# Kernel optimization log

Measured on AMD Instinct MI355X. Metric: run time of the kernel, lower is better.

## Reference

```python
import jax, jax.numpy as jnp
import numpy as np

EPS = 1e-5

def _bn(z, g, b):
    # train-mode BatchNorm2d: batch stats over (B,H,W), biased variance
    mean = z.mean(axis=(0, 2, 3), keepdims=True)
    var = z.var(axis=(0, 2, 3), keepdims=True)
    return g[None, :, None, None] * (z - mean) * jax.lax.rsqrt(var + EPS) + b[None, :, None, None]

def _conv1x1(x, w):
    # x: [B,C,H,W], w: [O,C] -> [B,O,H,W]
    return jnp.einsum('bchw,oc->bohw', x, w)

def _proj(x, w1, g1, b1, w2, g2, b2):
    z = _bn(_conv1x1(x, w1), g1, b1)
    return _bn(_conv1x1(z, w2), g2, b2)

def setup_inputs() -> dict:
    key = jax.random.key(0)
    ks = jax.random.split(key, 24)
    B, Cx, Cy, M, H, W = 4, 512, 256, 64, 64, 64
    f32 = jnp.float32
    def wmat(k, o, c):
        return jax.random.normal(k, (o, c), f32) * (c ** -0.5)
    def gamma(k, c):
        return 1.0 + 0.1 * jax.random.normal(k, (c,), f32)
    def beta(k, c):
        return 0.1 * jax.random.normal(k, (c,), f32)
    inp = {
        'x': jax.random.normal(ks[0], (B, Cx, H, W), f32),
        'y': jax.random.normal(ks[1], (B, Cy, H, W), f32),
        # f_self
        'ws1': wmat(ks[2], M, Cx), 'gs1': gamma(ks[3], M), 'bs1': beta(ks[4], M),
        'ws2': wmat(ks[5], M, M),  'gs2': gamma(ks[6], M), 'bs2': beta(ks[7], M),
        # f_x
        'wx1': wmat(ks[8], M, Cx), 'gx1': gamma(ks[9], M), 'bx1': beta(ks[10], M),
        'wx2': wmat(ks[11], M, M), 'gx2': gamma(ks[12], M), 'bx2': beta(ks[13], M),
        # f_y
        'wy1': wmat(ks[14], M, Cy), 'gy1': gamma(ks[15], M), 'by1': beta(ks[16], M),
        'wy2': wmat(ks[17], M, M),  'gy2': gamma(ks[18], M), 'by2': beta(ks[19], M),
        # f_up
        'wu': wmat(ks[20], Cx, M), 'gu': gamma(ks[21], Cx), 'bu': beta(ks[22], Cx),
    }
    return inp

def reference(x, y, ws1, gs1, bs1, ws2, gs2, bs2,
              wx1, gx1, bx1, wx2, gx2, bx2,
              wy1, gy1, by1, wy2, gy2, by2,
              wu, gu, bu):
    B, C, H, W = x.shape
    M = ws1.shape[0]
    N = H * W
    fself = _proj(x, ws1, gs1, bs1, ws2, gs2, bs2).reshape(B, M, N).transpose(0, 2, 1)  # [B,N,M]
    fx = _proj(x, wx1, gx1, bx1, wx2, gx2, bx2).reshape(B, M, N).transpose(0, 2, 1)      # [B,N,M]
    fy = _proj(y, wy1, gy1, by1, wy2, gy2, by2).reshape(B, M, N)                          # [B,M,N]
    sim = jnp.matmul(fx, fy)                  # [B,N,N]  (scale=False)
    attn = jax.nn.softmax(sim, axis=-1)
    fout = jnp.matmul(attn, fself)            # [B,N,M]
    fout = fout.transpose(0, 2, 1).reshape(B, M, H, W)
    out = _bn(_conv1x1(fout, wu), gu, bu)
    return x + out
```

## Files before the change

### kernel.cpp

```cpp
#include <hip/hip_runtime.h>
#include <hip/hip_fp16.h>
#include <cstdint>

constexpr int N_ = 4096;
constexpr float CNT = 16384.f;

typedef __attribute__((ext_vector_type(8))) _Float16 half8;
typedef __attribute__((ext_vector_type(4))) float f32x4;
union fragh { half8 h8; int i4[4]; };

__device__ inline int pkh(float a, float b) {
  union { __half2 h; int i; } u;
  u.h = __float22half2_rn(float2{a, b});
  return u.i;
}


__global__ __launch_bounds__(256) void prep1_k(const float* __restrict__ ws1,
                                               const float* __restrict__ wx1,
                                               const float* __restrict__ wy1,
                                               float* __restrict__ wt1) {
  int e = blockIdx.x * 256 + threadIdx.x;
  if (e < 32768) {
    int k = e >> 6, o = e & 63;
    wt1[e] = ws1[o * 512 + k];
  } else if (e < 65536) {
    int e2 = e - 32768;
    int k = e2 >> 6, o = e2 & 63;
    wt1[e] = wx1[o * 512 + k];
  } else {
    int e3 = e - 65536;
    int k = e3 >> 6, o = e3 & 63;
    wt1[e] = wy1[o * 256 + k];
  }
}

__global__ __launch_bounds__(256) void prep2_k(
    const float* __restrict__ ws2, const float* __restrict__ wx2,
    const float* __restrict__ wy2,
    const float* __restrict__ gs1, const float* __restrict__ bs1,
    const float* __restrict__ gx1, const float* __restrict__ bx1,
    const float* __restrict__ gy1, const float* __restrict__ by1,
    const float* __restrict__ stats, float* __restrict__ wt2) {
  const int branch = blockIdx.x;
  const int t = threadIdx.x;
  const float* W = branch == 0 ? ws2 : (branch == 1 ? wx2 : wy2);
  const float* g1 = branch == 0 ? gs1 : (branch == 1 ? gx1 : gy1);
  const float* b1 = branch == 0 ? bs1 : (branch == 1 ? bx1 : by1);
  const float* stin = stats + branch * 128;
  float* outW = wt2 + branch * 4096;
  float* outB = wt2 + 12288 + branch * 64;

#pragma unroll
  for (int i = 0; i < 16; ++i) {
    int e = i * 256 + t;
    int k = e >> 6, o = e & 63;
    float mean = stin[k] * (1.f / CNT);
    float var = stin[64 + k] * (1.f / CNT) - mean * mean;
    float sc = g1[k] * rsqrtf(var + 1e-5f);
    outW[e] = W[o * 64 + k] * sc;
  }
  if (t < 64) {
    float s = 0.f;
    for (int k = 0; k < 64; ++k) {
      float mean = stin[k] * (1.f / CNT);
      float var = stin[64 + k] * (1.f / CNT) - mean * mean;
      float sc = g1[k] * rsqrtf(var + 1e-5f);
      float sh = b1[k] - mean * sc;
      s += W[t * 64 + k] * sh;
    }
    outB[t] = s;
  }
}

__global__ __launch_bounds__(256) void prepu_k(const float* __restrict__ wu,
                                               float* __restrict__ wut) {
  int e = blockIdx.x * 256 + threadIdx.x;
  int k = e >> 9, o = e & 511;
  wut[e] = wu[o * 64 + k];
}


__global__ __launch_bounds__(256) void conv1_k(
    const float* __restrict__ x, const float* __restrict__ y,
    const float* __restrict__ wt1,
    float* __restrict__ z1s, float* __restrict__ z1x, float* __restrict__ z1y,
    float* __restrict__ stats) {
  const int t = threadIdx.x;
  const int b = blockIdx.x >> 4;
  const int n0 = (blockIdx.x & 15) * 256;
  const int branch = blockIdx.y;
  const float* A = branch == 2 ? y : x;
  const float* Wt = wt1 + (branch == 0 ? 0 : (branch == 1 ? 32768 : 65536));
  float* out = branch == 0 ? z1s : (branch == 1 ? z1x : z1y);
  const int K = branch == 2 ? 256 : 512;
  float* st = stats + branch * 128;

  __shared__ float sA[16][260];
  __shared__ float sW[16][68];

  const int ng4 = (t & 31) * 4;
  const int og8 = (t >> 5) * 8;
  float acc[8][8];
#pragma unroll
  for (int i = 0; i < 8; ++i)
#pragma unroll
    for (int j = 0; j < 8; ++j) acc[i][j] = 0.f;

  const float* Ap = A + ((size_t)b * K + (t >> 6)) * N_ + n0 + (t & 63) * 4;
  const float* Wp = Wt + (size_t)(t >> 4) * 64 + (t & 15) * 4;
  const int arow = t >> 6, acol = (t & 63) * 4;
  const int wrow = t >> 4, wcol = (t & 15) * 4;

  float4 pa[4];
  float4 pw;
#pragma unroll
  for (int i = 0; i < 4; ++i) pa[i] = *(const float4*)(Ap + (size_t)(4 * i) * N_);
  pw = *(const float4*)Wp;
  Ap += (size_t)16 * N_;
  Wp += 16 * 64;
#pragma unroll
  for (int i = 0; i < 4; ++i) *(float4*)&sA[arow + 4 * i][acol] = pa[i];
  *(float4*)&sW[wrow][wcol] = pw;
  __syncthreads();

#pragma unroll 1
  for (int k0 = 0; k0 < K; k0 += 16) {
    const bool more = (k0 + 16) < K;
    if (more) {
#pragma unroll
      for (int i = 0; i < 4; ++i) pa[i] = *(const float4*)(Ap + (size_t)(4 * i) * N_);
      pw = *(const float4*)Wp;
      Ap += (size_t)16 * N_;
      Wp += 16 * 64;
    }
#pragma unroll
    for (int k = 0; k < 16; ++k) {
      float4 a0 = *(const float4*)&sA[k][ng4];
      float4 a1 = *(const float4*)&sA[k][128 + ng4];
      float4 w0 = *(const float4*)&sW[k][og8];
      float4 w1 = *(const float4*)&sW[k][og8 + 4];
      float av[8] = {a0.x, a0.y, a0.z, a0.w, a1.x, a1.y, a1.z, a1.w};
      float wv[8] = {w0.x, w0.y, w0.z, w0.w, w1.x, w1.y, w1.z, w1.w};
#pragma unroll
      for (int i = 0; i < 8; ++i)
#pragma unroll
        for (int j = 0; j < 8; ++j) acc[i][j] = fmaf(wv[i], av[j], acc[i][j]);
    }
    __syncthreads();
    if (more) {
#pragma unroll
      for (int i = 0; i < 4; ++i) *(float4*)&sA[arow + 4 * i][acol] = pa[i];
      *(float4*)&sW[wrow][wcol] = pw;
    }
    __syncthreads();
  }

  float* Cb = out + ((size_t)b * 64 + og8) * N_ + n0;
#pragma unroll
  for (int i = 0; i < 8; ++i) {
    float4 v0 = {acc[i][0], acc[i][1], acc[i][2], acc[i][3]};
    float4 v1 = {acc[i][4], acc[i][5], acc[i][6], acc[i][7]};
    *(float4*)&Cb[(size_t)i * N_ + ng4] = v0;
    *(float4*)&Cb[(size_t)i * N_ + 128 + ng4] = v1;
  }
#pragma unroll
  for (int i = 0; i < 8; ++i) {
    float s = 0.f, q = 0.f;
#pragma unroll
    for (int j = 0; j < 8; ++j) { s += acc[i][j]; q += acc[i][j] * acc[i][j]; }
#pragma unroll
    for (int d = 1; d < 32; d <<= 1) { s += __shfl_xor(s, d); q += __shfl_xor(q, d); }
    if ((t & 31) == 0) { atomicAdd(&st[og8 + i], s); atomicAdd(&st[64 + og8 + i], q); }
  }
}

__global__ __launch_bounds__(256) void conv2_k(
    const float* __restrict__ z1s, const float* __restrict__ z1x,
    const float* __restrict__ z1y, const float* __restrict__ wt2,
    float* __restrict__ z2s, float* __restrict__ z2x, float* __restrict__ z2y,
    float* __restrict__ stats) {
  const int t = threadIdx.x;
  const int b = blockIdx.x >> 4;
  const int n0 = (blockIdx.x & 15) * 256;
  const int branch = blockIdx.y;
  const float* A = branch == 0 ? z1s : (branch == 1 ? z1x : z1y);
  const float* Wt = wt2 + branch * 4096;
  const float* bias = wt2 + 12288 + branch * 64;
  float* out = branch == 0 ? z2s : (branch == 1 ? z2x : z2y);
  float* st = stats + (3 + branch) * 128;

  __shared__ float sA[16][260];
  __shared__ float sW[16][68];

  const int ng4 = (t & 31) * 4;
  const int og8 = (t >> 5) * 8;
  float acc[8][8];
#pragma unroll
  for (int i = 0; i < 8; ++i) {
    float bi = bias[og8 + i];
#pragma unroll
    for (int j = 0; j < 8; ++j) acc[i][j] = bi;
  }

  const float* Ap = A + ((size_t)b * 64 + (t >> 6)) * N_ + n0 + (t & 63) * 4;
  const float* Wp = Wt + (size_t)(t >> 4) * 64 + (t & 15) * 4;
  const int arow = t >> 6, acol = (t & 63) * 4;
  const int wrow = t >> 4, wcol = (t & 15) * 4;

  float4 pa[4];
  float4 pw;
#pragma unroll
  for (int i = 0; i < 4; ++i) pa[i] = *(const float4*)(Ap + (size_t)(4 * i) * N_);
  pw = *(const float4*)Wp;
  Ap += (size_t)16 * N_;
  Wp += 16 * 64;
#pragma unroll
  for (int i = 0; i < 4; ++i) *(float4*)&sA[arow + 4 * i][acol] = pa[i];
  *(float4*)&sW[wrow][wcol] = pw;
  __syncthreads();

#pragma unroll 1
  for (int k0 = 0; k0 < 64; k0 += 16) {
    const bool more = (k0 + 16) < 64;
    if (more) {
#pragma unroll
      for (int i = 0; i < 4; ++i) pa[i] = *(const float4*)(Ap + (size_t)(4 * i) * N_);
      pw = *(const float4*)Wp;
      Ap += (size_t)16 * N_;
      Wp += 16 * 64;
    }
#pragma unroll
    for (int k = 0; k < 16; ++k) {
      float4 a0 = *(const float4*)&sA[k][ng4];
      float4 a1 = *(const float4*)&sA[k][128 + ng4];
      float4 w0 = *(const float4*)&sW[k][og8];
      float4 w1 = *(const float4*)&sW[k][og8 + 4];
      float av[8] = {a0.x, a0.y, a0.z, a0.w, a1.x, a1.y, a1.z, a1.w};
      float wv[8] = {w0.x, w0.y, w0.z, w0.w, w1.x, w1.y, w1.z, w1.w};
#pragma unroll
      for (int i = 0; i < 8; ++i)
#pragma unroll
        for (int j = 0; j < 8; ++j) acc[i][j] = fmaf(wv[i], av[j], acc[i][j]);
    }
    __syncthreads();
    if (more) {
#pragma unroll
      for (int i = 0; i < 4; ++i) *(float4*)&sA[arow + 4 * i][acol] = pa[i];
      *(float4*)&sW[wrow][wcol] = pw;
    }
    __syncthreads();
  }

  float* Cb = out + ((size_t)b * 64 + og8) * N_ + n0;
#pragma unroll
  for (int i = 0; i < 8; ++i) {
    float4 v0 = {acc[i][0], acc[i][1], acc[i][2], acc[i][3]};
    float4 v1 = {acc[i][4], acc[i][5], acc[i][6], acc[i][7]};
    *(float4*)&Cb[(size_t)i * N_ + ng4] = v0;
    *(float4*)&Cb[(size_t)i * N_ + 128 + ng4] = v1;
  }
#pragma unroll
  for (int i = 0; i < 8; ++i) {
    float s = 0.f, q = 0.f;
#pragma unroll
    for (int j = 0; j < 8; ++j) { s += acc[i][j]; q += acc[i][j] * acc[i][j]; }
#pragma unroll
    for (int d = 1; d < 32; d <<= 1) { s += __shfl_xor(s, d); q += __shfl_xor(q, d); }
    if ((t & 31) == 0) { atomicAdd(&st[og8 + i], s); atomicAdd(&st[64 + og8 + i], q); }
  }
}

__global__ __launch_bounds__(256) void pack_k(
    const float* __restrict__ z2s, const float* __restrict__ z2x,
    const float* __restrict__ z2y,
    const float* __restrict__ gs2, const float* __restrict__ bs2,
    const float* __restrict__ gx2, const float* __restrict__ bx2,
    const float* __restrict__ gy2, const float* __restrict__ by2,
    int* __restrict__ Qh, int* __restrict__ Kf, int* __restrict__ Vf,
    const float* __restrict__ stats) {
  const int job = blockIdx.z;
  const int idx = blockIdx.x * 256 + threadIdx.x;
  const float* z2 = job == 0 ? z2x : (job == 1 ? z2y : z2s);
  const float* g2 = job == 0 ? gx2 : (job == 1 ? gy2 : gs2);
  const float* b2 = job == 0 ? bx2 : (job == 1 ? by2 : bs2);
  const float* st = stats + (job == 0 ? 4 : (job == 1 ? 5 : 3)) * 128;
  int* outp = job == 0 ? Qh : (job == 1 ? Kf : Vf);

  auto snorm = [&](int c, float& s, float& h) {
    float mean = st[c] * (1.f / CNT);
    float var = st[64 + c] * (1.f / CNT) - mean * mean;
    float r = rsqrtf(var + 1e-5f);
    s = g2[c] * r;
    h = b2[c] - mean * s;
  };
  if (job == 0) {
    int n = idx & 4095, c = (idx >> 12) & 31, b = idx >> 17;
    float s0, h0, s1, h1;
    snorm(2 * c, s0, h0);
    snorm(2 * c + 1, s1, h1);
    float v0 = z2[((size_t)b * 64 + 2 * c) * N_ + n] * s0 + h0;
    float v1 = z2[((size_t)b * 64 + 2 * c + 1) * N_ + n] * s1 + h1;
    outp[idx] = pkh(v0, v1);
  } else if (job == 1) {
    int n = idx & 4095, c = (idx >> 12) & 31, b = idx >> 17;
    float s0, h0, s1, h1;
    snorm(2 * c, s0, h0);
    snorm(2 * c + 1, s1, h1);
    float v0 = z2[((size_t)b * 64 + 2 * c) * N_ + n] * s0 + h0;
    float v1 = z2[((size_t)b * 64 + 2 * c + 1) * N_ + n] * s1 + h1;
    int t16 = n >> 4, la = n & 15, g = c >> 4, quad = (c & 15) >> 2, jj = c & 3;
    outp[(((b * 256 + t16) * 2 + g) * 64 + quad * 16 + la) * 4 + jj] = pkh(v0, v1);
  } else {
    int k = idx & 2047, ch = (idx >> 11) & 63, b = idx >> 17;
    float s0, h0;
    snorm(ch, s0, h0);
    float2 v = *(const float2*)&z2[((size_t)b * 64 + ch) * N_ + 2 * k];
    int kb = k >> 4, p = k & 15, quad = p >> 2, w = p & 3, mt = ch >> 4, la = ch & 15;
    outp[(((b * 128 + kb) * 4 + mt) * 64 + quad * 16 + la) * 4 + w] =
        pkh(v.x * s0 + h0, v.y * s0 + h0);
  }
}

__global__ __launch_bounds__(256, 4) void attn_k(const int* __restrict__ Qh,
                                                 const int* __restrict__ Kf,
                                                 const int* __restrict__ Vf,
                                                 float* __restrict__ fout) {
  const int tid = threadIdx.x;
  const int lane = tid & 63;
  const int wid = tid >> 6;
  const int la = lane & 15;
  const int quad = lane >> 4;
  const int b = blockIdx.x & 3;
  const int qbase = (blockIdx.x >> 2) * 16;
  const int* Qb = Qh + (size_t)b * 32 * N_;
  const int* Kb4 = Kf + (size_t)b * 131072;
  const int* Vb4 = Vf + (size_t)b * 131072;

  __shared__ union USm {
    int P16[4][16 * 20];
    struct { float O[4][16][69]; float M[4][16]; float L[4][16]; } e;
  } smu;
  int* myP = smu.P16[wid];

  fragh aq[2];
#pragma unroll
  for (int c = 0; c < 2; ++c)
#pragma unroll
    for (int j = 0; j < 4; ++j)
      aq[c].i4[j] = Qb[(size_t)(c * 16 + quad * 4 + j) * N_ + qbase + la];

  f32x4 o[4];
  float mrun = -3.0e38f, lrun = 0.f;
#pragma unroll
  for (int mt = 0; mt < 4; ++mt) o[mt] = f32x4{0.f, 0.f, 0.f, 0.f};

  const int jbeg = wid * (N_ / 4);
  const int jend = jbeg + N_ / 4;

  int4 ka[2][2], kb2[2][2];
#pragma unroll
  for (int nt = 0; nt < 2; ++nt)
#pragma unroll
    for (int g = 0; g < 2; ++g)
      ka[nt][g] = *(const int4*)&Kb4[((((jbeg >> 4) + nt) * 2 + g) * 64 + lane) * 4];

  auto body = [&](int j0, int4 (&kc)[2][2], int4 (&kn)[2][2]) {
    f32x4 s[2];
#pragma unroll
    for (int nt = 0; nt < 2; ++nt) {
      fragh k0, k1;
      k0.i4[0] = kc[nt][0].x; k0.i4[1] = kc[nt][0].y;
      k0.i4[2] = kc[nt][0].z; k0.i4[3] = kc[nt][0].w;
      k1.i4[0] = kc[nt][1].x; k1.i4[1] = kc[nt][1].y;
      k1.i4[2] = kc[nt][1].z; k1.i4[3] = kc[nt][1].w;
      f32x4 z = f32x4{0.f, 0.f, 0.f, 0.f};
      z = __builtin_amdgcn_mfma_f32_16x16x32_f16(k0.h8, aq[0].h8, z, 0, 0, 0);
      s[nt] = __builtin_amdgcn_mfma_f32_16x16x32_f16(k1.h8, aq[1].h8, z, 0, 0, 0);
    }
    int4 vv[4];
#pragma unroll
    for (int mt = 0; mt < 4; ++mt)
      vv[mt] = *(const int4*)&Vb4[(((j0 >> 5) * 4 + mt) * 64 + lane) * 4];
    const int nj = (j0 + 32 < jend) ? (j0 + 32) : jbeg;
#pragma unroll
    for (int nt = 0; nt < 2; ++nt)
#pragma unroll
      for (int g = 0; g < 2; ++g)
        kn[nt][g] = *(const int4*)&Kb4[((((nj >> 4) + nt) * 2 + g) * 64 + lane) * 4];
    float t0 = fmaxf(fmaxf(s[0][0], s[0][1]), fmaxf(s[0][2], s[0][3]));
    float t1 = fmaxf(fmaxf(s[1][0], s[1][1]), fmaxf(s[1][2], s[1][3]));
    float t = fmaxf(t0, t1);
    t = fmaxf(t, __shfl_xor(t, 16));
    t = fmaxf(t, __shfl_xor(t, 32));
    float mnew = fmaxf(mrun, t);
    float alpha = __expf(mrun - mnew);
    float p[2][4];
    float ps = 0.f;
#pragma unroll
    for (int nt = 0; nt < 2; ++nt)
#pragma unroll
      for (int r = 0; r < 4; ++r) {
        p[nt][r] = __expf(s[nt][r] - mnew);
        ps += p[nt][r];
      }
    ps += __shfl_xor(ps, 16);
    ps += __shfl_xor(ps, 32);
    lrun = lrun * alpha + ps;
    mrun = mnew;
#pragma unroll
    for (int nt = 0; nt < 2; ++nt) {
      myP[(nt * 8 + quad * 2 + 0) * 20 + la] = pkh(p[nt][0], p[nt][1]);
      myP[(nt * 8 + quad * 2 + 1) * 20 + la] = pkh(p[nt][2], p[nt][3]);
    }
    __asm__ __volatile__("s_waitcnt lgkmcnt(0)" ::: "memory");
    fragh pb;
#pragma unroll
    for (int j = 0; j < 4; ++j) pb.i4[j] = myP[(quad * 4 + j) * 20 + la];
#pragma unroll
    for (int mt = 0; mt < 4; ++mt) {
      o[mt][0] *= alpha; o[mt][1] *= alpha;
      o[mt][2] *= alpha; o[mt][3] *= alpha;
    }
#pragma unroll
    for (int mt = 0; mt < 4; ++mt) {
      fragh vb;
      vb.i4[0] = vv[mt].x; vb.i4[1] = vv[mt].y;
      vb.i4[2] = vv[mt].z; vb.i4[3] = vv[mt].w;
      o[mt] = __builtin_amdgcn_mfma_f32_16x16x32_f16(vb.h8, pb.h8, o[mt], 0, 0, 0);
    }
  };

#pragma unroll 1
  for (int j0 = jbeg; j0 < jend; j0 += 64) {
    body(j0, ka, kb2);
    body(j0 + 32, kb2, ka);
  }

  __syncthreads();
  if (quad == 0) {
    smu.e.M[wid][la] = mrun;
    smu.e.L[wid][la] = lrun;
  }
#pragma unroll
  for (int mt = 0; mt < 4; ++mt)
#pragma unroll
    for (int r = 0; r < 4; ++r) smu.e.O[wid][la][mt * 16 + quad * 4 + r] = o[mt][r];
  __syncthreads();

#pragma unroll
  for (int t = 0; t < 4; ++t) {
    int oidx = t * 256 + tid;
    int m = oidx >> 4;
    int q = oidx & 15;
    float m0 = fmaxf(fmaxf(smu.e.M[0][q], smu.e.M[1][q]),
                     fmaxf(smu.e.M[2][q], smu.e.M[3][q]));
    float num = 0.f, den = 0.f;
#pragma unroll
    for (int w = 0; w < 4; ++w) {
      float wgt = __expf(smu.e.M[w][q] - m0);
      num += wgt * smu.e.O[w][q][m];
      den += wgt * smu.e.L[w][q];
    }
    fout[((size_t)b * 64 + m) * N_ + qbase + q] = num / den;
  }
}

__global__ __launch_bounds__(256) void convup_k(const float* __restrict__ fout,
                                                const float* __restrict__ wut,
                                                float* __restrict__ u,
                                                float* __restrict__ stats) {
  const int t = threadIdx.x;
  const int b = blockIdx.x >> 4;
  const int n0 = (blockIdx.x & 15) * 256;
  const int o0 = blockIdx.y * 64;

  __shared__ float sA[16][260];
  __shared__ float sW[16][68];

  const int ng4 = (t & 31) * 4;
  const int og8 = (t >> 5) * 8;
  float acc[8][8];
#pragma unroll
  for (int i = 0; i < 8; ++i)
#pragma unroll
    for (int j = 0; j < 8; ++j) acc[i][j] = 0.f;

  const float* Ap = fout + ((size_t)b * 64 + (t >> 6)) * N_ + n0 + (t & 63) * 4;
  const float* Wp = wut + (size_t)(t >> 4) * 512 + o0 + (t & 15) * 4;
  const int arow = t >> 6, acol = (t & 63) * 4;
  const int wrow = t >> 4, wcol = (t & 15) * 4;

  float4 pa[4];
  float4 pw;
#pragma unroll
  for (int i = 0; i < 4; ++i) pa[i] = *(const float4*)(Ap + (size_t)(4 * i) * N_);
  pw = *(const float4*)Wp;
  Ap += (size_t)16 * N_;
  Wp += 16 * 512;
#pragma unroll
  for (int i = 0; i < 4; ++i) *(float4*)&sA[arow + 4 * i][acol] = pa[i];
  *(float4*)&sW[wrow][wcol] = pw;
  __syncthreads();

#pragma unroll 1
  for (int k0 = 0; k0 < 64; k0 += 16) {
    const bool more = (k0 + 16) < 64;
    if (more) {
#pragma unroll
      for (int i = 0; i < 4; ++i) pa[i] = *(const float4*)(Ap + (size_t)(4 * i) * N_);
      pw = *(const float4*)Wp;
      Ap += (size_t)16 * N_;
      Wp += 16 * 512;
    }
#pragma unroll
    for (int k = 0; k < 16; ++k) {
      float4 a0 = *(const float4*)&sA[k][ng4];
      float4 a1 = *(const float4*)&sA[k][128 + ng4];
      float4 w0 = *(const float4*)&sW[k][og8];
      float4 w1 = *(const float4*)&sW[k][og8 + 4];
      float av[8] = {a0.x, a0.y, a0.z, a0.w, a1.x, a1.y, a1.z, a1.w};
      float wv[8] = {w0.x, w0.y, w0.z, w0.w, w1.x, w1.y, w1.z, w1.w};
#pragma unroll
      for (int i = 0; i < 8; ++i)
#pragma unroll
        for (int j = 0; j < 8; ++j) acc[i][j] = fmaf(wv[i], av[j], acc[i][j]);
    }
    __syncthreads();
    if (more) {
#pragma unroll
      for (int i = 0; i < 4; ++i) *(float4*)&sA[arow + 4 * i][acol] = pa[i];
      *(float4*)&sW[wrow][wcol] = pw;
    }
    __syncthreads();
  }

  float* Cb = u + ((size_t)b * 512 + o0 + og8) * N_ + n0;
#pragma unroll
  for (int i = 0; i < 8; ++i) {
    float4 v0 = {acc[i][0], acc[i][1], acc[i][2], acc[i][3]};
    float4 v1 = {acc[i][4], acc[i][5], acc[i][6], acc[i][7]};
    *(float4*)&Cb[(size_t)i * N_ + ng4] = v0;
    *(float4*)&Cb[(size_t)i * N_ + 128 + ng4] = v1;
  }
#pragma unroll
  for (int i = 0; i < 8; ++i) {
    float s = 0.f, q = 0.f;
#pragma unroll
    for (int j = 0; j < 8; ++j) { s += acc[i][j]; q += acc[i][j] * acc[i][j]; }
#pragma unroll
    for (int d = 1; d < 32; d <<= 1) { s += __shfl_xor(s, d); q += __shfl_xor(q, d); }
    if ((t & 31) == 0) {
      atomicAdd(&stats[768 + o0 + og8 + i], s);
      atomicAdd(&stats[1280 + o0 + og8 + i], q);
    }
  }
}

__global__ __launch_bounds__(256) void final_k(const float* __restrict__ x,
                                               const float* __restrict__ u,
                                               const float* __restrict__ gu,
                                               const float* __restrict__ bu,
                                               const float* __restrict__ stats,
                                               float* __restrict__ out) {
  size_t idx = (size_t)blockIdx.x * 256 + threadIdx.x;
  int c = (int)((idx >> 12) & 511);
  float mean = stats[768 + c] * (1.f / CNT);
  float var = stats[1280 + c] * (1.f / CNT) - mean * mean;
  float r = rsqrtf(var + 1e-5f);
  float s = gu[c] * r;
  float sh = bu[c] - mean * s;
  out[idx] = x[idx] + u[idx] * s + sh;
}

extern "C" void kernel_launch(void* const* d_in, const int* in_sizes, int n_in,
                              void* d_out, int out_size, void* d_ws, size_t ws_size,
                              hipStream_t stream) {
  const float* x = (const float*)d_in[0];
  const float* y = (const float*)d_in[1];
  const float* ws1 = (const float*)d_in[2];
  const float* gs1 = (const float*)d_in[3];
  const float* bs1 = (const float*)d_in[4];
  const float* ws2 = (const float*)d_in[5];
  const float* gs2 = (const float*)d_in[6];
  const float* bs2 = (const float*)d_in[7];
  const float* wx1 = (const float*)d_in[8];
  const float* gx1 = (const float*)d_in[9];
  const float* bx1 = (const float*)d_in[10];
  const float* wx2 = (const float*)d_in[11];
  const float* gx2 = (const float*)d_in[12];
  const float* bx2 = (const float*)d_in[13];
  const float* wy1 = (const float*)d_in[14];
  const float* gy1 = (const float*)d_in[15];
  const float* by1 = (const float*)d_in[16];
  const float* wy2 = (const float*)d_in[17];
  const float* gy2 = (const float*)d_in[18];
  const float* by2 = (const float*)d_in[19];
  const float* wu = (const float*)d_in[20];
  const float* gu = (const float*)d_in[21];
  const float* bu = (const float*)d_in[22];
  float* out = (float*)d_out;

  float* w = (float*)d_ws;
  const size_t M1 = 1048576;
  float* z1s = w + 0 * M1;
  float* z1x = w + 1 * M1;
  float* z1y = w + 2 * M1;
  float* z2s = w + 3 * M1;
  float* z2x = w + 4 * M1;
  float* z2y = w + 5 * M1;
  float* fout = w + 6 * M1;
  float* u = w + 7 * M1;
  int* Qh = (int*)(w + 15 * M1);
  int* Kf = Qh + 524288;
  int* Vf = Kf + 524288;
  float* stats = (float*)(Vf + 524288);
  float* wt1 = u;
  float* wt2 = fout;
  float* wut = z1s;

  hipMemsetAsync(stats, 0, 1792 * sizeof(float), stream);

  prep1_k<<<dim3(320), dim3(256), 0, stream>>>(ws1, wx1, wy1, wt1);
  conv1_k<<<dim3(64, 3), dim3(256), 0, stream>>>(x, y, wt1, z1s, z1x, z1y, stats);
  prep2_k<<<dim3(3), dim3(256), 0, stream>>>(ws2, wx2, wy2, gs1, bs1, gx1, bx1,
                                             gy1, by1, stats, wt2);
  conv2_k<<<dim3(64, 3), dim3(256), 0, stream>>>(z1s, z1x, z1y, wt2, z2s, z2x,
                                                 z2y, stats);
  prepu_k<<<dim3(128), dim3(256), 0, stream>>>(wu, wut);
  pack_k<<<dim3(2048, 1, 3), dim3(256), 0, stream>>>(z2s, z2x, z2y, gs2, bs2, gx2,
                                                     bx2, gy2, by2, Qh, Kf, Vf,
                                                     stats);
  attn_k<<<dim3(1024), dim3(256), 0, stream>>>(Qh, Kf, Vf, fout);
  convup_k<<<dim3(64, 8), dim3(256), 0, stream>>>(fout, wut, u, stats);
  final_k<<<dim3(32768), dim3(256), 0, stream>>>(x, u, gu, bu, stats, out);
}
```

Before: 378.6 us.

## Move 1x1 projection convs to split-fp16 MFMA with fragment-packed layouts

Rewrites conv1 and conv2 to use fp16 MFMA instructions. Each fp32 value is split into high and low half parts, and three MFMAs per tile stand in for the scalar FP32 FMA loop with LDS tiling. A new packA kernel converts x and y into MFMA fragment layout. Intermediates z1/z2 are stored as hi/lo half pairs in fragment order, so pack_k and attn_k now read Q and K in the new layout. This trades an extra packing pass over the inputs and the error of the hi/lo split for much higher matrix throughput in the projection GEMMs.

```diff
diff --git a/kernel.cpp b/kernel.cpp
--- a/kernel.cpp
+++ b/kernel.cpp
@@ -14,25 +14,70 @@
   u.h = __float22half2_rn(float2{a, b});
   return u.i;
 }
-
+__device__ inline void pk_hl(float a, float b, int& h, int& l) {
+  __half ah = __float2half_rn(a), bh = __float2half_rn(b);
+  union { __half2 v; int i; } u;
+  u.v = __halves2half2(ah, bh);
+  h = u.i;
+  float ar = a - __half2float(ah), br = b - __half2float(bh);
+  union { __half2 v; int i; } w2;
+  w2.v = __float22half2_rn(float2{ar, br});
+  l = w2.i;
+}
+__device__ inline float2 uph(int v) {
+  union { __half2 h; int i; } u;
+  u.i = v;
+  return float2{__half2float(__low2half(u.h)), __half2float(__high2half(u.h))};
+}
+
+
+__global__ __launch_bounds__(256) void packA_k(const float* __restrict__ x,
+                                               const float* __restrict__ y,
+                                               int* __restrict__ Afx,
+                                               int* __restrict__ Afy) {
+  const int job = blockIdx.y;
+  if (job == 1 && blockIdx.x >= 2048) return;
+  const int idx = blockIdx.x * 256 + threadIdx.x;
+  const float* src = job ? y : x;
+  int* dst = job ? Afy : Afx;
+  const int KT = job ? 8 : 16;
+  const int loOff = job ? 2097152 : 4194304;
+  const int n = idx & 4095, q = (idx >> 12) & 3;
+  const int kt = job ? ((idx >> 14) & 7) : ((idx >> 14) & 15);
+  const int b = job ? (idx >> 17) : (idx >> 18);
+  const float* sp = src + ((size_t)(b * (KT * 32) + kt * 32 + q * 8)) * N_ + n;
+  float a[8];
+#pragma unroll
+  for (int j = 0; j < 8; ++j) a[j] = sp[(size_t)j * N_];
+  int4 hi, lo;
+  pk_hl(a[0], a[1], hi.x, lo.x);
+  pk_hl(a[2], a[3], hi.y, lo.y);
+  pk_hl(a[4], a[5], hi.z, lo.z);
+  pk_hl(a[6], a[7], hi.w, lo.w);
+  const int base = (((b * KT + kt) * 256 + (n >> 4)) * 64 + q * 16 + (n & 15)) * 4;
+  *(int4*)&dst[base] = hi;
+  *(int4*)&dst[loOff + base] = lo;
+}
 
 __global__ __launch_bounds__(256) void prep1_k(const float* __restrict__ ws1,
                                                const float* __restrict__ wx1,
                                                const float* __restrict__ wy1,
-                                               float* __restrict__ wt1) {
-  int e = blockIdx.x * 256 + threadIdx.x;
-  if (e < 32768) {
-    int k = e >> 6, o = e & 63;
-    wt1[e] = ws1[o * 512 + k];
-  } else if (e < 65536) {
-    int e2 = e - 32768;
-    int k = e2 >> 6, o = e2 & 63;
-    wt1[e] = wx1[o * 512 + k];
-  } else {
-    int e3 = e - 65536;
-    int k = e3 >> 6, o = e3 & 63;
-    wt1[e] = wy1[o * 256 + k];
-  }
+                                               int* __restrict__ wt1f) {
+  const int idx = blockIdx.x * 256 + threadIdx.x;
+  const float* W;
+  int KT, K, hiBase, loOff, e;
+  if (idx < 16384) { W = ws1; KT = 16; K = 512; hiBase = 0; loOff = 16384; e = idx; }
+  else if (idx < 32768) { W = wx1; KT = 16; K = 512; hiBase = 32768; loOff = 16384; e = idx - 16384; }
+  else { W = wy1; KT = 8; K = 256; hiBase = 65536; loOff = 8192; e = idx - 32768; }
+  const int jj = e & 3, lane = (e >> 2) & 63;
+  int kt, ot;
+  if (KT == 16) { kt = (e >> 8) & 15; ot = e >> 12; } else { kt = (e >> 8) & 7; ot = e >> 11; }
+  const int o = ot * 16 + (lane & 15);
+  const int k = kt * 32 + (lane >> 4) * 8 + 2 * jj;
+  int h, l;
+  pk_hl(W[o * K + k], W[o * K + k + 1], h, l);
+  wt1f[hiBase + e] = h;
+  wt1f[hiBase + loOff + e] = l;
 }
 
 __global__ __launch_bounds__(256) void prep2_k(
@@ -41,24 +86,33 @@
     const float* __restrict__ gs1, const float* __restrict__ bs1,
     const float* __restrict__ gx1, const float* __restrict__ bx1,
     const float* __restrict__ gy1, const float* __restrict__ by1,
-    const float* __restrict__ stats, float* __restrict__ wt2) {
+    const float* __restrict__ stats, int* __restrict__ wt2f,
+    float* __restrict__ biasf) {
   const int branch = blockIdx.x;
   const int t = threadIdx.x;
   const float* W = branch == 0 ? ws2 : (branch == 1 ? wx2 : wy2);
   const float* g1 = branch == 0 ? gs1 : (branch == 1 ? gx1 : gy1);
   const float* b1 = branch == 0 ? bs1 : (branch == 1 ? bx1 : by1);
   const float* stin = stats + branch * 128;
-  float* outW = wt2 + branch * 4096;
-  float* outB = wt2 + 12288 + branch * 64;
-
-#pragma unroll
-  for (int i = 0; i < 16; ++i) {
-    int e = i * 256 + t;
-    int k = e >> 6, o = e & 63;
+  int* outW = wt2f + branch * 4096;
+
+  auto scale = [&](int k) {
     float mean = stin[k] * (1.f / CNT);
     float var = stin[64 + k] * (1.f / CNT) - mean * mean;
-    float sc = g1[k] * rsqrtf(var + 1e-5f);
-    outW[e] = W[o * 64 + k] * sc;
+    return g1[k] * rsqrtf(var + 1e-5f);
+  };
+#pragma unroll
+  for (int i = 0; i < 8; ++i) {
+    int e = i * 256 + t;
+    int jj = e & 3, lane = (e >> 2) & 63, kt = (e >> 8) & 1, ot = e >> 9;
+    int o = ot * 16 + (lane & 15);
+    int k = kt * 32 + (lane >> 4) * 8 + 2 * jj;
+    float w0 = W[o * 64 + k] * scale(k);
+    float w1 = W[o * 64 + k + 1] * scale(k + 1);
+    int h, l;
+    pk_hl(w0, w1, h, l);
+    outW[e] = h;
+    outW[2048 + e] = l;
   }
   if (t < 64) {
     float s = 0.f;
@@ -69,7 +123,7 @@
       float sh = b1[k] - mean * sc;
       s += W[t * 64 + k] * sh;
     }
-    outB[t] = s;
+    biasf[branch * 64 + t] = s;
   }
 }
 
@@ -80,212 +134,183 @@
   wut[e] = wu[o * 64 + k];
 }
 
-
 __global__ __launch_bounds__(256) void conv1_k(
-    const float* __restrict__ x, const float* __restrict__ y,
-    const float* __restrict__ wt1,
-    float* __restrict__ z1s, float* __restrict__ z1x, float* __restrict__ z1y,
+    const int* __restrict__ Afx, const int* __restrict__ Afy,
+    const int* __restrict__ wt1f, int* __restrict__ z1f,
     float* __restrict__ stats) {
   const int t = threadIdx.x;
+  const int lane = t & 63;
+  const int wv = t >> 6;
+  const int la = lane & 15;
+  const int quad = lane >> 4;
   const int b = blockIdx.x >> 4;
-  const int n0 = (blockIdx.x & 15) * 256;
+  const int ns = blockIdx.x & 15;
   const int branch = blockIdx.y;
-  const float* A = branch == 2 ? y : x;
-  const float* Wt = wt1 + (branch == 0 ? 0 : (branch == 1 ? 32768 : 65536));
-  float* out = branch == 0 ? z1s : (branch == 1 ? z1x : z1y);
-  const int K = branch == 2 ? 256 : 512;
+  const int KT = branch == 2 ? 8 : 16;
+  const int* Af = branch == 2 ? Afy : Afx;
+  const int aLo = branch == 2 ? 2097152 : 4194304;
+  const int* Wf = wt1f + (branch == 0 ? 0 : (branch == 1 ? 32768 : 65536));
+  const int wLo = branch == 2 ? 8192 : 16384;
   float* st = stats + branch * 128;
-
-  __shared__ float sA[16][260];
-  __shared__ float sW[16][68];
-
-  const int ng4 = (t & 31) * 4;
-  const int og8 = (t >> 5) * 8;
-  float acc[8][8];
-#pragma unroll
-  for (int i = 0; i < 8; ++i)
-#pragma unroll
-    for (int j = 0; j < 8; ++j) acc[i][j] = 0.f;
-
-  const float* Ap = A + ((size_t)b * K + (t >> 6)) * N_ + n0 + (t & 63) * 4;
-  const float* Wp = Wt + (size_t)(t >> 4) * 64 + (t & 15) * 4;
-  const int arow = t >> 6, acol = (t & 63) * 4;
-  const int wrow = t >> 4, wcol = (t & 15) * 4;
-
-  float4 pa[4];
-  float4 pw;
-#pragma unroll
-  for (int i = 0; i < 4; ++i) pa[i] = *(const float4*)(Ap + (size_t)(4 * i) * N_);
-  pw = *(const float4*)Wp;
-  Ap += (size_t)16 * N_;
-  Wp += 16 * 64;
-#pragma unroll
-  for (int i = 0; i < 4; ++i) *(float4*)&sA[arow + 4 * i][acol] = pa[i];
-  *(float4*)&sW[wrow][wcol] = pw;
-  __syncthreads();
-
+  int* zb = z1f + branch * 1048576;
+
+  f32x4 acc[4][4];
+#pragma unroll
+  for (int i = 0; i < 4; ++i)
+#pragma unroll
+    for (int j = 0; j < 4; ++j) acc[i][j] = f32x4{0.f, 0.f, 0.f, 0.f};
+
+  const int ntg0 = ns * 16 + wv * 4;
 #pragma unroll 1
-  for (int k0 = 0; k0 < K; k0 += 16) {
-    const bool more = (k0 + 16) < K;
-    if (more) {
-#pragma unroll
-      for (int i = 0; i < 4; ++i) pa[i] = *(const float4*)(Ap + (size_t)(4 * i) * N_);
-      pw = *(const float4*)Wp;
-      Ap += (size_t)16 * N_;
-      Wp += 16 * 64;
-    }
-#pragma unroll
-    for (int k = 0; k < 16; ++k) {
-      float4 a0 = *(const float4*)&sA[k][ng4];
-      float4 a1 = *(const float4*)&sA[k][128 + ng4];
-      float4 w0 = *(const float4*)&sW[k][og8];
-      float4 w1 = *(const float4*)&sW[k][og8 + 4];
-      float av[8] = {a0.x, a0.y, a0.z, a0.w, a1.x, a1.y, a1.z, a1.w};
-      float wv[8] = {w0.x, w0.y, w0.z, w0.w, w1.x, w1.y, w1.z, w1.w};
-#pragma unroll
-      for (int i = 0; i < 8; ++i)
-#pragma unroll
-        for (int j = 0; j < 8; ++j) acc[i][j] = fmaf(wv[i], av[j], acc[i][j]);
-    }
-    __syncthreads();
-    if (more) {
-#pragma unroll
-      for (int i = 0; i < 4; ++i) *(float4*)&sA[arow + 4 * i][acol] = pa[i];
-      *(float4*)&sW[wrow][wcol] = pw;
-    }
-    __syncthreads();
-  }
-
-  float* Cb = out + ((size_t)b * 64 + og8) * N_ + n0;
-#pragma unroll
-  for (int i = 0; i < 8; ++i) {
-    float4 v0 = {acc[i][0], acc[i][1], acc[i][2], acc[i][3]};
-    float4 v1 = {acc[i][4], acc[i][5], acc[i][6], acc[i][7]};
-    *(float4*)&Cb[(size_t)i * N_ + ng4] = v0;
-    *(float4*)&Cb[(size_t)i * N_ + 128 + ng4] = v1;
-  }
-#pragma unroll
-  for (int i = 0; i < 8; ++i) {
-    float s = 0.f, q = 0.f;
-#pragma unroll
-    for (int j = 0; j < 8; ++j) { s += acc[i][j]; q += acc[i][j] * acc[i][j]; }
-#pragma unroll
-    for (int d = 1; d < 32; d <<= 1) { s += __shfl_xor(s, d); q += __shfl_xor(q, d); }
-    if ((t & 31) == 0) { atomicAdd(&st[og8 + i], s); atomicAdd(&st[64 + og8 + i], q); }
-  }
+  for (int kt = 0; kt < KT; ++kt) {
+    fragh wh[4], wl[4], ah[4], al[4];
+#pragma unroll
+    for (int ot = 0; ot < 4; ++ot) {
+      const int base = ((ot * KT + kt) * 64 + lane) * 4;
+      *(int4*)wh[ot].i4 = *(const int4*)&Wf[base];
+      *(int4*)wl[ot].i4 = *(const int4*)&Wf[wLo + base];
+    }
+#pragma unroll
+    for (int nt = 0; nt < 4; ++nt) {
+      const int base = (((b * KT + kt) * 256 + ntg0 + nt) * 64 + lane) * 4;
+      *(int4*)ah[nt].i4 = *(const int4*)&Af[base];
+      *(int4*)al[nt].i4 = *(const int4*)&Af[aLo + base];
+    }
+#pragma unroll
+    for (int ot = 0; ot < 4; ++ot)
+#pragma unroll
+      for (int nt = 0; nt < 4; ++nt) {
+        acc[ot][nt] = __builtin_amdgcn_mfma_f32_16x16x32_f16(wh[ot].h8, ah[nt].h8, acc[ot][nt], 0, 0, 0);
+        acc[ot][nt] = __builtin_amdgcn_mfma_f32_16x16x32_f16(wh[ot].h8, al[nt].h8, acc[ot][nt], 0, 0, 0);
+        acc[ot][nt] = __builtin_amdgcn_mfma_f32_16x16x32_f16(wl[ot].h8, ah[nt].h8, acc[ot][nt], 0, 0, 0);
+      }
+  }
+#pragma unroll
+  for (int ot = 0; ot < 4; ++ot) {
+    const int ktz = ot >> 1;
+    const int qz = (ot & 1) * 2 + (quad >> 1);
+    const int jz = (quad & 1) * 2;
+#pragma unroll
+    for (int nt = 0; nt < 4; ++nt) {
+      const int addr = (((b * 2 + ktz) * 256 + ntg0 + nt) * 64 + qz * 16 + la) * 4 + jz;
+      int h0, l0, h1, l1;
+      pk_hl(acc[ot][nt][0], acc[ot][nt][1], h0, l0);
+      pk_hl(acc[ot][nt][2], acc[ot][nt][3], h1, l1);
+      *(int2*)&zb[addr] = int2{h0, h1};
+      *(int2*)&zb[524288 + addr] = int2{l0, l1};
+    }
+  }
+#pragma unroll
+  for (int ot = 0; ot < 4; ++ot)
+#pragma unroll
+    for (int r = 0; r < 4; ++r) {
+      float s = acc[ot][0][r] + acc[ot][1][r] + acc[ot][2][r] + acc[ot][3][r];
+      float q = acc[ot][0][r] * acc[ot][0][r] + acc[ot][1][r] * acc[ot][1][r] +
+                acc[ot][2][r] * acc[ot][2][r] + acc[ot][3][r] * acc[ot][3][r];
+#pragma unroll
+      for (int d = 1; d < 16; d <<= 1) { s += __shfl_xor(s, d); q += __shfl_xor(q, d); }
+      if (la == 0) {
+        atomicAdd(&st[ot * 16 + quad * 4 + r], s);
+        atomicAdd(&st[64 + ot * 16 + quad * 4 + r], q);
+      }
+    }
 }
 
 __global__ __launch_bounds__(256) void conv2_k(
-    const float* __restrict__ z1s, const float* __restrict__ z1x,
-    const float* __restrict__ z1y, const float* __restrict__ wt2,
-    float* __restrict__ z2s, float* __restrict__ z2x, float* __restrict__ z2y,
+    const int* __restrict__ z1f, const int* __restrict__ wt2f,
+    const float* __restrict__ biasf, int* __restrict__ z2f,
     float* __restrict__ stats) {
   const int t = threadIdx.x;
+  const int lane = t & 63;
+  const int wv = t >> 6;
+  const int la = lane & 15;
+  const int quad = lane >> 4;
   const int b = blockIdx.x >> 4;
-  const int n0 = (blockIdx.x & 15) * 256;
+  const int ns = blockIdx.x & 15;
   const int branch = blockIdx.y;
-  const float* A = branch == 0 ? z1s : (branch == 1 ? z1x : z1y);
-  const float* Wt = wt2 + branch * 4096;
-  const float* bias = wt2 + 12288 + branch * 64;
-  float* out = branch == 0 ? z2s : (branch == 1 ? z2x : z2y);
+  const int* Af = z1f + branch * 1048576;
+  const int* Wf = wt2f + branch * 4096;
+  const float* bias = biasf + branch * 64;
   float* st = stats + (3 + branch) * 128;
-
-  __shared__ float sA[16][260];
-  __shared__ float sW[16][68];
-
-  const int ng4 = (t & 31) * 4;
-  const int og8 = (t >> 5) * 8;
-  float acc[8][8];
-#pragma unroll
-  for (int i = 0; i < 8; ++i) {
-    float bi = bias[og8 + i];
-#pragma unroll
-    for (int j = 0; j < 8; ++j) acc[i][j] = bi;
-  }
-
-  const float* Ap = A + ((size_t)b * 64 + (t >> 6)) * N_ + n0 + (t & 63) * 4;
-  const float* Wp = Wt + (size_t)(t >> 4) * 64 + (t & 15) * 4;
-  const int arow = t >> 6, acol = (t & 63) * 4;
-  const int wrow = t >> 4, wcol = (t & 15) * 4;
-
-  float4 pa[4];
-  float4 pw;
-#pragma unroll
-  for (int i = 0; i < 4; ++i) pa[i] = *(const float4*)(Ap + (size_t)(4 * i) * N_);
-  pw = *(const float4*)Wp;
-  Ap += (size_t)16 * N_;
-  Wp += 16 * 64;
-#pragma unroll
-  for (int i = 0; i < 4; ++i) *(float4*)&sA[arow + 4 * i][acol] = pa[i];
-  *(float4*)&sW[wrow][wcol] = pw;
-  __syncthreads();
-
+  int* zb = z2f + branch * 1048576;
+
+  f32x4 acc[4][4];
+#pragma unroll
+  for (int ot = 0; ot < 4; ++ot)
+#pragma unroll
+    for (int nt = 0; nt < 4; ++nt) {
+#pragma unroll
+      for (int r = 0; r < 4; ++r) acc[ot][nt][r] = bias[ot * 16 + quad * 4 + r];
+    }
+
+  const int ntg0 = ns * 16 + wv * 4;
 #pragma unroll 1
-  for (int k0 = 0; k0 < 64; k0 += 16) {
-    const bool more = (k0 + 16) < 64;
-    if (more) {
-#pragma unroll
-      for (int i = 0; i < 4; ++i) pa[i] = *(const float4*)(Ap + (size_t)(4 * i) * N_);
-      pw = *(const float4*)Wp;
-      Ap += (size_t)16 * N_;
-      Wp += 16 * 64;
-    }
-#pragma unroll
-    for (int k = 0; k < 16; ++k) {
-      float4 a0 = *(const float4*)&sA[k][ng4];
-      float4 a1 = *(const float4*)&sA[k][128 + ng4];
-      float4 w0 = *(const float4*)&sW[k][og8];
-      float4 w1 = *(const float4*)&sW[k][og8 + 4];
-      float av[8] = {a0.x, a0.y, a0.z, a0.w, a1.x, a1.y, a1.z, a1.w};
-      float wv[8] = {w0.x, w0.y, w0.z, w0.w, w1.x, w1.y, w1.z, w1.w};
-#pragma unroll
-      for (int i = 0; i < 8; ++i)
-#pragma unroll
-        for (int j = 0; j < 8; ++j) acc[i][j] = fmaf(wv[i], av[j], acc[i][j]);
-    }
-    __syncthreads();
-    if (more) {
-#pragma unroll
-      for (int i = 0; i < 4; ++i) *(float4*)&sA[arow + 4 * i][acol] = pa[i];
-      *(float4*)&sW[wrow][wcol] = pw;
-    }
-    __syncthreads();
-  }
-
-  float* Cb = out + ((size_t)b * 64 + og8) * N_ + n0;
-#pragma unroll
-  for (int i = 0; i < 8; ++i) {
-    float4 v0 = {acc[i][0], acc[i][1], acc[i][2], acc[i][3]};
-    float4 v1 = {acc[i][4], acc[i][5], acc[i][6], acc[i][7]};
-    *(float4*)&Cb[(size_t)i * N_ + ng4] = v0;
-    *(float4*)&Cb[(size_t)i * N_ + 128 + ng4] = v1;
-  }
-#pragma unroll
-  for (int i = 0; i < 8; ++i) {
-    float s = 0.f, q = 0.f;
-#pragma unroll
-    for (int j = 0; j < 8; ++j) { s += acc[i][j]; q += acc[i][j] * acc[i][j]; }
-#pragma unroll
-    for (int d = 1; d < 32; d <<= 1) { s += __shfl_xor(s, d); q += __shfl_xor(q, d); }
-    if ((t & 31) == 0) { atomicAdd(&st[og8 + i], s); atomicAdd(&st[64 + og8 + i], q); }
-  }
+  for (int kt = 0; kt < 2; ++kt) {
+    fragh wh[4], wl[4], ah[4], al[4];
+#pragma unroll
+    for (int ot = 0; ot < 4; ++ot) {
+      const int base = ((ot * 2 + kt) * 64 + lane) * 4;
+      *(int4*)wh[ot].i4 = *(const int4*)&Wf[base];
+      *(int4*)wl[ot].i4 = *(const int4*)&Wf[2048 + base];
+    }
+#pragma unroll
+    for (int nt = 0; nt < 4; ++nt) {
+      const int base = (((b * 2 + kt) * 256 + ntg0 + nt) * 64 + lane) * 4;
+      *(int4*)ah[nt].i4 = *(const int4*)&Af[base];
+      *(int4*)al[nt].i4 = *(const int4*)&Af[524288 + base];
+    }
+#pragma unroll
+    for (int ot = 0; ot < 4; ++ot)
+#pragma unroll
+      for (int nt = 0; nt < 4; ++nt) {
+        acc[ot][nt] = __builtin_amdgcn_mfma_f32_16x16x32_f16(wh[ot].h8, ah[nt].h8, acc[ot][nt], 0, 0, 0);
+        acc[ot][nt] = __builtin_amdgcn_mfma_f32_16x16x32_f16(wh[ot].h8, al[nt].h8, acc[ot][nt], 0, 0, 0);
+        acc[ot][nt] = __builtin_amdgcn_mfma_f32_16x16x32_f16(wl[ot].h8, ah[nt].h8, acc[ot][nt], 0, 0, 0);
+      }
+  }
+#pragma unroll
+  for (int ot = 0; ot < 4; ++ot) {
+    const int ktz = ot >> 1;
+    const int qz = (ot & 1) * 2 + (quad >> 1);
+    const int jz = (quad & 1) * 2;
+#pragma unroll
+    for (int nt = 0; nt < 4; ++nt) {
+      const int addr = (((b * 2 + ktz) * 256 + ntg0 + nt) * 64 + qz * 16 + la) * 4 + jz;
+      int h0, l0, h1, l1;
+      pk_hl(acc[ot][nt][0], acc[ot][nt][1], h0, l0);
+      pk_hl(acc[ot][nt][2], acc[ot][nt][3], h1, l1);
+      *(int2*)&zb[addr] = int2{h0, h1};
+      *(int2*)&zb[524288 + addr] = int2{l0, l1};
+    }
+  }
+#pragma unroll
+  for (int ot = 0; ot < 4; ++ot)
+#pragma unroll
+    for (int r = 0; r < 4; ++r) {
+      float s = acc[ot][0][r] + acc[ot][1][r] + acc[ot][2][r] + acc[ot][3][r];
+      float q = acc[ot][0][r] * acc[ot][0][r] + acc[ot][1][r] * acc[ot][1][r] +
+                acc[ot][2][r] * acc[ot][2][r] + acc[ot][3][r] * acc[ot][3][r];
+#pragma unroll
+      for (int d = 1; d < 16; d <<= 1) { s += __shfl_xor(s, d); q += __shfl_xor(q, d); }
+      if (la == 0) {
+        atomicAdd(&st[ot * 16 + quad * 4 + r], s);
+        atomicAdd(&st[64 + ot * 16 + quad * 4 + r], q);
+      }
+    }
 }
 
 __global__ __launch_bounds__(256) void pack_k(
-    const float* __restrict__ z2s, const float* __restrict__ z2x,
-    const float* __restrict__ z2y,
+    const int* __restrict__ z2f,
     const float* __restrict__ gs2, const float* __restrict__ bs2,
     const float* __restrict__ gx2, const float* __restrict__ bx2,
     const float* __restrict__ gy2, const float* __restrict__ by2,
-    int* __restrict__ Qh, int* __restrict__ Kf, int* __restrict__ Vf,
+    int* __restrict__ Qf, int* __restrict__ Kf, int* __restrict__ Vf,
     const float* __restrict__ stats) {
   const int job = blockIdx.z;
   const int idx = blockIdx.x * 256 + threadIdx.x;
-  const float* z2 = job == 0 ? z2x : (job == 1 ? z2y : z2s);
   const float* g2 = job == 0 ? gx2 : (job == 1 ? gy2 : gs2);
   const float* b2 = job == 0 ? bx2 : (job == 1 ? by2 : bs2);
   const float* st = stats + (job == 0 ? 4 : (job == 1 ? 5 : 3)) * 128;
-  int* outp = job == 0 ? Qh : (job == 1 ? Kf : Vf);
 
   auto snorm = [&](int c, float& s, float& h) {
     float mean = st[c] * (1.f / CNT);
@@ -294,35 +319,37 @@
     s = g2[c] * r;
     h = b2[c] - mean * s;
   };
-  if (job == 0) {
-    int n = idx & 4095, c = (idx >> 12) & 31, b = idx >> 17;
+  if (job < 2) {
+    const int* zf = z2f + (job == 0 ? 1048576 : 2097152);
+    int* outp = job == 0 ? Qf : Kf;
+    int h = zf[idx], l = zf[524288 + idx];
+    int jj = idx & 3, lane = (idx >> 2) & 63, q = lane >> 4;
+    int kt = (idx >> 16) & 1;
+    int c0 = 2 * (kt * 16 + q * 4 + jj);
     float s0, h0, s1, h1;
-    snorm(2 * c, s0, h0);
-    snorm(2 * c + 1, s1, h1);
-    float v0 = z2[((size_t)b * 64 + 2 * c) * N_ + n] * s0 + h0;
-    float v1 = z2[((size_t)b * 64 + 2 * c + 1) * N_ + n] * s1 + h1;
-    outp[idx] = pkh(v0, v1);
-  } else if (job == 1) {
-    int n = idx & 4095, c = (idx >> 12) & 31, b = idx >> 17;
-    float s0, h0, s1, h1;
-    snorm(2 * c, s0, h0);
-    snorm(2 * c + 1, s1, h1);
-    float v0 = z2[((size_t)b * 64 + 2 * c) * N_ + n] * s0 + h0;
-    float v1 = z2[((size_t)b * 64 + 2 * c + 1) * N_ + n] * s1 + h1;
-    int t16 = n >> 4, la = n & 15, g = c >> 4, quad = (c & 15) >> 2, jj = c & 3;
-    outp[(((b * 256 + t16) * 2 + g) * 64 + quad * 16 + la) * 4 + jj] = pkh(v0, v1);
+    snorm(c0, s0, h0);
+    snorm(c0 + 1, s1, h1);
+    float2 vh = uph(h), vl = uph(l);
+    outp[idx] = pkh((vh.x + vl.x) * s0 + h0, (vh.y + vl.y) * s1 + h1);
   } else {
-    int k = idx & 2047, ch = (idx >> 11) & 63, b = idx >> 17;
+    int w_ = idx & 3, lane = (idx >> 2) & 63, la_v = lane & 15, q_v = lane >> 4;
+    int mt = (idx >> 8) & 3, kb = (idx >> 10) & 127, b = idx >> 17;
+    int ch = mt * 16 + la_v;
+    int k = kb * 16 + q_v * 4 + w_;
+    int n0 = 2 * k;
+    int kp = ch >> 1, kt = kp >> 4, qz = (kp >> 2) & 3, jz = kp & 3, half = ch & 1;
+    int a0 = (((b * 2 + kt) * 256 + (n0 >> 4)) * 64 + qz * 16 + (n0 & 15)) * 4 + jz;
+    float2 h0v = uph(z2f[a0]), l0v = uph(z2f[524288 + a0]);
+    float2 h1v = uph(z2f[a0 + 4]), l1v = uph(z2f[524288 + a0 + 4]);
+    float v0 = half ? (h0v.y + l0v.y) : (h0v.x + l0v.x);
+    float v1 = half ? (h1v.y + l1v.y) : (h1v.x + l1v.x);
     float s0, h0;
     snorm(ch, s0, h0);
-    float2 v = *(const float2*)&z2[((size_t)b * 64 + ch) * N_ + 2 * k];
-    int kb = k >> 4, p = k & 15, quad = p >> 2, w = p & 3, mt = ch >> 4, la = ch & 15;
-    outp[(((b * 128 + kb) * 4 + mt) * 64 + quad * 16 + la) * 4 + w] =
-        pkh(v.x * s0 + h0, v.y * s0 + h0);
-  }
-}
-
-__global__ __launch_bounds__(256, 4) void attn_k(const int* __restrict__ Qh,
+    Vf[idx] = pkh(v0 * s0 + h0, v1 * s0 + h0);
+  }
+}
+
+__global__ __launch_bounds__(256, 4) void attn_k(const int* __restrict__ Qf,
                                                  const int* __restrict__ Kf,
                                                  const int* __restrict__ Vf,
                                                  float* __restrict__ fout) {
@@ -333,7 +360,7 @@
   const int quad = lane >> 4;
   const int b = blockIdx.x & 3;
   const int qbase = (blockIdx.x >> 2) * 16;
-  const int* Qb = Qh + (size_t)b * 32 * N_;
+  const int* Qb = Qf + (size_t)b * 131072;
   const int* Kb4 = Kf + (size_t)b * 131072;
   const int* Vb4 = Vf + (size_t)b * 131072;
 
@@ -346,9 +373,8 @@
   fragh aq[2];
 #pragma unroll
   for (int c = 0; c < 2; ++c)
-#pragma unroll
-    for (int j = 0; j < 4; ++j)
-      aq[c].i4[j] = Qb[(size_t)(c * 16 + quad * 4 + j) * N_ + qbase + la];
+    *(int4*)aq[c].i4 =
+        *(const int4*)&Qb[((c * 256 + (qbase >> 4)) * 64 + quad * 16 + la) * 4];
 
   f32x4 o[4];
   float mrun = -3.0e38f, lrun = 0.f;
@@ -363,7 +389,7 @@
   for (int nt = 0; nt < 2; ++nt)
 #pragma unroll
     for (int g = 0; g < 2; ++g)
-      ka[nt][g] = *(const int4*)&Kb4[((((jbeg >> 4) + nt) * 2 + g) * 64 + lane) * 4];
+      ka[nt][g] = *(const int4*)&Kb4[((g * 256 + (jbeg >> 4) + nt) * 64 + lane) * 4];
 
   auto body = [&](int j0, int4 (&kc)[2][2], int4 (&kn)[2][2]) {
     f32x4 s[2];
@@ -387,7 +413,7 @@
     for (int nt = 0; nt < 2; ++nt)
 #pragma unroll
       for (int g = 0; g < 2; ++g)
-        kn[nt][g] = *(const int4*)&Kb4[((((nj >> 4) + nt) * 2 + g) * 64 + lane) * 4];
+        kn[nt][g] = *(const int4*)&Kb4[((g * 256 + (nj >> 4) + nt) * 64 + lane) * 4];
     float t0 = fmaxf(fmaxf(s[0][0], s[0][1]), fmaxf(s[0][2], s[0][3]));
     float t1 = fmaxf(fmaxf(s[1][0], s[1][1]), fmaxf(s[1][2], s[1][3]));
     float t = fmaxf(t0, t1);
@@ -603,35 +629,33 @@
 
   float* w = (float*)d_ws;
   const size_t M1 = 1048576;
-  float* z1s = w + 0 * M1;
-  float* z1x = w + 1 * M1;
-  float* z1y = w + 2 * M1;
-  float* z2s = w + 3 * M1;
-  float* z2x = w + 4 * M1;
-  float* z2y = w + 5 * M1;
+  int* z1f = (int*)w;
+  int* z2f = (int*)(w + 3 * M1);
   float* fout = w + 6 * M1;
   float* u = w + 7 * M1;
-  int* Qh = (int*)(w + 15 * M1);
-  int* Kf = Qh + 524288;
+  int* Afx = (int*)u;
+  int* Afy = (int*)(w + 3 * M1);
+  int* Qf = (int*)(w + 15 * M1);
+  int* Kf = Qf + 524288;
   int* Vf = Kf + 524288;
   float* stats = (float*)(Vf + 524288);
-  float* wt1 = u;
-  float* wt2 = fout;
-  float* wut = z1s;
+  int* wt1f = (int*)(stats + 1792);
+  int* wt2f = wt1f + 81920;
+  float* biasf = (float*)(wt2f + 12288);
+  float* wut = biasf + 192;
 
   hipMemsetAsync(stats, 0, 1792 * sizeof(float), stream);
 
-  prep1_k<<<dim3(320), dim3(256), 0, stream>>>(ws1, wx1, wy1, wt1);
-  conv1_k<<<dim3(64, 3), dim3(256), 0, stream>>>(x, y, wt1, z1s, z1x, z1y, stats);
+  prep1_k<<<dim3(160), dim3(256), 0, stream>>>(ws1, wx1, wy1, wt1f);
+  packA_k<<<dim3(4096, 2), dim3(256), 0, stream>>>(x, y, Afx, Afy);
+  conv1_k<<<dim3(64, 3), dim3(256), 0, stream>>>(Afx, Afy, wt1f, z1f, stats);
   prep2_k<<<dim3(3), dim3(256), 0, stream>>>(ws2, wx2, wy2, gs1, bs1, gx1, bx1,
-                                             gy1, by1, stats, wt2);
-  conv2_k<<<dim3(64, 3), dim3(256), 0, stream>>>(z1s, z1x, z1y, wt2, z2s, z2x,
-                                                 z2y, stats);
+                                             gy1, by1, stats, wt2f, biasf);
+  conv2_k<<<dim3(64, 3), dim3(256), 0, stream>>>(z1f, wt2f, biasf, z2f, stats);
   prepu_k<<<dim3(128), dim3(256), 0, stream>>>(wu, wut);
-  pack_k<<<dim3(2048, 1, 3), dim3(256), 0, stream>>>(z2s, z2x, z2y, gs2, bs2, gx2,
-                                                     bx2, gy2, by2, Qh, Kf, Vf,
-                                                     stats);
-  attn_k<<<dim3(1024), dim3(256), 0, stream>>>(Qh, Kf, Vf, fout);
+  pack_k<<<dim3(2048, 1, 3), dim3(256), 0, stream>>>(z2f, gs2, bs2, gx2, bx2, gy2,
+                                                     by2, Qf, Kf, Vf, stats);
+  attn_k<<<dim3(1024), dim3(256), 0, stream>>>(Qf, Kf, Vf, fout);
   convup_k<<<dim3(64, 8), dim3(256), 0, stream>>>(fout, wut, u, stats);
   final_k<<<dim3(32768), dim3(256), 0, stream>>>(x, u, gu, bu, stats, out);
 }
```

Result: faster. 368.5 us (-2.7%).
